# Optimization experiments

Hardware: AMD Instinct MI355X
Metric: run time of the kernel (lower is better)

## Reference

```python
import jax, jax.numpy as jnp
import numpy as np

KSIZE = 3
KN = (KSIZE - 1) // 2  # 1
TEMP = 50.0


def _extract_patches(x, same_pad):
    """TF tf.image.extract_patches ordering: per location, (dy, dx, channel).
    x: [b,H,W,d] -> [b,h,w,9*d] (h=H,w=W if same_pad else H-2,W-2)."""
    if same_pad:
        x = jnp.pad(x, ((0, 0), (KN, KN), (KN, KN), (0, 0)))
    b, Hp, Wp, d = x.shape
    h, w = Hp - 2 * KN, Wp - 2 * KN
    slices = [x[:, dy:dy + h, dx:dx + w, :]
              for dy in range(KSIZE) for dx in range(KSIZE)]
    return jnp.concatenate(slices, axis=-1)


def setup_inputs() -> dict:
    key = jax.random.key(0)
    k1, k2, k3 = jax.random.split(key, 3)
    b, h, w, dims = 4, 48, 48, 64
    g_in = jax.random.normal(k1, (b, h, w, dims), dtype=jnp.float32)
    # binary inpainting mask (1 = known background, 0 = hole)
    mask = (jax.random.uniform(k2, (b, h, w, 1)) > 0.5).astype(jnp.float32)
    W2 = jax.random.normal(k3, (2 * dims, dims), dtype=jnp.float32) / np.sqrt(2.0 * dims)
    b2 = jnp.zeros((dims,), dtype=jnp.float32)
    return {"g_in": g_in, "mask": mask, "W2": W2, "b2": b2}


def reference(g_in, mask, W2, b2):
    b, h, w, dims = g_in.shape
    c = (h - 2 * KN) * (w - 2 * KN)

    mask_r = mask  # already (h,w,1); broadcasts over dims (== tile)
    bg = g_in * mask_r

    # p1: VALID 3x3 patches of bg -> dynamic kernels, [b, c, 9*dims]
    p1 = _extract_patches(bg, same_pad=False).reshape(b, c, KSIZE * KSIZE * dims)
    # p2: SAME 3x3 patches of g_in, [b, h, w, 9*dims]
    p2 = _extract_patches(g_in, same_pad=True)

    # cross-correlation: conv2d(ft, k1) == per-location dot with each bg patch
    CS = jnp.einsum('byxk,bjk->byxj', p2, p1)              # [b,h,w,c]
    k1d = jnp.sum(p1 * p1, axis=2)                          # [b,c]
    wwd = jnp.sum(p2 * p2, axis=3, keepdims=True)           # [b,h,w,1]
    DS1 = k1d[:, None, None, :] + wwd - 2.0 * CS            # squared distances
    mu = jnp.mean(DS1, axis=3, keepdims=True)
    sd = jnp.std(DS1, axis=3, keepdims=True)                # population std (tf.math.reduce_std)
    DS2 = -jnp.tanh((DS1 - mu) / sd)
    CA = jax.nn.softmax(TEMP * DS2, axis=-1)                # [b,h,w,c]

    # transposed conv aggregation with per-sample kernels k2[b,j,dy,dx,ch]
    k2 = p1.reshape(b, c, KSIZE, KSIZE, dims)
    CA_pad = jnp.pad(CA, ((0, 0), (KN, KN), (KN, KN), (0, 0)))
    acl = jnp.zeros((b, h, w, dims), dtype=g_in.dtype)
    for dy in range(KSIZE):
        for dx in range(KSIZE):
            win = CA_pad[:, 2 * KN - dy:2 * KN - dy + h, 2 * KN - dx:2 * KN - dx + w, :]
            acl = acl + jnp.einsum('byxj,bjd->byxd', win, k2[:, :, dy, dx, :])
    acl = acl / 9.0

    ACL = bg + acl * (1.0 - mask_r)
    con1 = jnp.concatenate([g_in, ACL], axis=3)             # [b,h,w,2*dims]
    return jax.nn.elu(jnp.einsum('byxk,kd->byxd', con1, W2) + b2)
```

## Files before the change

kernel.cpp:

```cpp
#include <hip/hip_runtime.h>
#include <hip/hip_fp16.h>
#include <math.h>

#define BB 4
#define HH 48
#define WW 48
#define DD 64
#define CH 46
#define CWp 46
#define CC (CH*CWp)
#define KK 576
#define HWp (HH*WW)
#define PW 50
#define PP (PW*PW)

#define SLOTW 48
#define NSLOT 2208
#define NGRP 276
#define KPAD NSLOT
#define KSPLIT0 1120
#define QW 2304
#define QROWS 2500

typedef __attribute__((ext_vector_type(8))) short short8;
typedef __attribute__((ext_vector_type(4))) float float4v;

#define OFFB_GPAD  ((size_t)0)
#define OFFB_BGPAD ((size_t)1280000)
#define OFFB_E     ((size_t)2560000)
#define OFFB_K1D   ((size_t)2596864)
#define OFFB_P1T   ((size_t)2632192)
#define OFFB_S     ((size_t)12806656)
#define OFFB_AGG0  ((size_t)53504512)
#define OFFB_AGG1  ((size_t)64121344)
#define OFFB_Q     ((size_t)74738176)

__device__ __forceinline__ ushort f2bf(float x) {
    unsigned u = __float_as_uint(x);
    return (ushort)((u + 0x7FFFu + ((u >> 16) & 1u)) >> 16);
}

__device__ __forceinline__ float waveReduceSum(float x) {
#pragma unroll
    for (int o = 32; o > 0; o >>= 1) x += __shfl_down(x, o, 64);
    return x;
}

__device__ __forceinline__ float blockReduce5(float x, float* sm) {
#pragma unroll
    for (int o = 32; o > 0; o >>= 1) x += __shfl_down(x, o, 64);
    int lane = threadIdx.x & 63, w = threadIdx.x >> 6;
    __syncthreads();
    if (lane == 0) sm[w] = x;
    __syncthreads();
    return sm[0] + sm[1] + sm[2] + sm[3] + sm[4];
}

__device__ __forceinline__ float fast_tanh(float z) {
    float e = __expf(2.f * z);
    return 1.f - 2.f / (e + 1.f);
}

typedef __attribute__((address_space(3))) void lds_void_t;
typedef __attribute__((address_space(1))) void gmem_void_t;
__device__ __forceinline__ void gld16(const ushort* g, ushort* lds) {
    __builtin_amdgcn_global_load_lds((gmem_void_t*)g, (lds_void_t*)lds, 16, 0, 0);
}

__global__ __launch_bounds__(256) void build_pads(const float* __restrict__ g,
                                                  const float* __restrict__ mask,
                                                  ushort* __restrict__ gpad,
                                                  ushort* __restrict__ bgpad,
                                                  float* __restrict__ e) {
    int w = threadIdx.x >> 6, c = threadIdx.x & 63;
    int q4 = blockIdx.x * 4 + w;
    int b = q4 / PP, q = q4 % PP;
    int yp = q / PW, xp = q % PW;
    size_t o = (size_t)q4 * DD + c;
    if (yp >= 1 && yp <= HH && xp >= 1 && xp <= WW) {
        int pix = (yp - 1) * WW + (xp - 1);
        float gv = g[((size_t)b * HWp + pix) * DD + c];
        float m  = mask[(size_t)b * HWp + pix];
        float bgv = gv * m;
        gpad[o]  = f2bf(gv);
        bgpad[o] = f2bf(bgv);
        float ss = waveReduceSum(bgv * bgv);
        if (c == 0) e[b * HWp + pix] = ss;
    } else {
        gpad[o] = 0;
        bgpad[o] = 0;
    }
}

__global__ __launch_bounds__(256) void build_p1t(const ushort* __restrict__ bgpad,
                                                 const float* __restrict__ e,
                                                 ushort* __restrict__ p1t,
                                                 float* __restrict__ k1d) {
    int d9 = blockIdx.y, b = blockIdx.z;
    int t = threadIdx.x;
    if (blockIdx.x == 35) {
        int jg = (b * 9 + d9) * 256 + t;
        if (jg < BB * NSLOT) {
            int bb = jg / NSLOT, st = jg - bb * NSLOT;
            int jy = st / SLOTW, jx = st - jy * SLOTW;
            float s = 0.f;
            if (jx < CWp) {
                const float* eb = e + bb * HWp + jy * WW + jx;
#pragma unroll
                for (int ddy = 0; ddy < 3; ddy++)
#pragma unroll
                    for (int ddx = 0; ddx < 3; ddx++) s += eb[ddy * WW + ddx];
            }
            k1d[jg] = s;
        }
        return;
    }
    __shared__ ushort T[64 * 65];
    int jt = blockIdx.x;
    int dy = d9 / 3, dx = d9 - dy * 3;
    const ushort* src = bgpad + (size_t)b * PP * DD;
    int lr = t >> 3, c8 = (t & 7) * 8;
#pragma unroll
    for (int pass = 0; pass < 2; pass++) {
        int r = lr + pass * 32;
        int st = jt * 64 + r;
        int jy = st / SLOTW, jx = st - jy * SLOTW;
        uint4 d = make_uint4(0, 0, 0, 0);
        if (jx < CWp && jy < CWp)
            d = *(const uint4*)(src + (size_t)((jy + dy + 1) * PW + (jx + dx + 1)) * DD + c8);
        ushort tmp[8];
        *(uint4*)tmp = d;
#pragma unroll
        for (int u = 0; u < 8; u++) T[r * 65 + c8 + u] = tmp[u];
    }
    __syncthreads();
#pragma unroll
    for (int pass = 0; pass < 2; pass++) {
        int c = lr + pass * 32;
        int j8 = (t & 7) * 8;
        int col0 = jt * 64 + j8;
        ushort tmp[8];
#pragma unroll
        for (int u = 0; u < 8; u++) tmp[u] = T[(j8 + u) * 65 + c];
        if (col0 < NSLOT)
            *(uint4*)(p1t + ((size_t)b * KK + d9 * 64 + c) * NSLOT + col0) = *(const uint4*)tmp;
    }
}

__global__ __launch_bounds__(256) void qgemm(const ushort* __restrict__ gpad,
                                             const ushort* __restrict__ bgpad,
                                             __half* __restrict__ Qout) {
    __shared__ ushort As[2 * 4096];
    __shared__ ushort Bs[2 * 4096];
    int i0 = blockIdx.x;
    int b = (i0 & 7) >> 1;
    int tile = ((i0 >> 3) << 1) | (i0 & 1);
    int ty = tile / 18, tx = tile - ty * 18;
    int m0 = ty * 128, n0 = tx * 128;
    const ushort* Ag = gpad + (size_t)b * PP * DD;
    const ushort* Bg = bgpad + (size_t)b * PP * DD;

    int tid = threadIdx.x;
    int l = tid & 63, w = tid >> 6;
    int quad = l >> 4, l15 = l & 15;
    int sw8 = (l15 >> 1) & 3;
    int wm = (w >> 1) * 64, wn = (w & 1) * 64;
    int rowInC = l >> 2;
    int cSw = (l & 3) ^ ((l >> 3) & 3);

#pragma unroll
    for (int i = 0; i < 2; i++) {
        int rg = w * 2 + i;
        int r = rg * 16 + rowInC;
        int u = m0 + r; if (u > QROWS - 1) u = QROWS - 1;
        int n = n0 + r;
        int vy = n / 48, vx = n - vy * 48;
        int baseA = u * DD + cSw * 8;
        int baseB = ((vy + 1) * PW + (vx + 1)) * DD + cSw * 8;
        gld16(Ag + baseA, As + rg * 512);
        gld16(Bg + baseB, Bs + rg * 512);
        gld16(Ag + baseA + 32, As + 4096 + rg * 512);
        gld16(Bg + baseB + 32, Bs + 4096 + rg * 512);
    }
    float4v acc[4][4];
#pragma unroll
    for (int i = 0; i < 4; i++)
#pragma unroll
        for (int j = 0; j < 4; j++) acc[i][j] = (float4v){0.f, 0.f, 0.f, 0.f};
    __syncthreads();
#pragma unroll
    for (int kb = 0; kb < 2; kb++) {
        const ushort* Ax = As + kb * 4096;
        const ushort* Bx = Bs + kb * 4096;
        short8 af[4], bf[4];
#pragma unroll
        for (int i = 0; i < 4; i++)
            af[i] = *(const short8*)&Ax[(wm + i * 16 + l15) * 32 + ((quad ^ sw8)) * 8];
#pragma unroll
        for (int j = 0; j < 4; j++)
            bf[j] = *(const short8*)&Bx[(wn + j * 16 + l15) * 32 + ((quad ^ sw8)) * 8];
#pragma unroll
        for (int i = 0; i < 4; i++)
#pragma unroll
            for (int j = 0; j < 4; j++)
                acc[i][j] = __builtin_amdgcn_mfma_f32_16x16x32_bf16(af[i], bf[j], acc[i][j], 0, 0, 0);
    }
    __half* C = Qout + (size_t)b * QROWS * QW;
#pragma unroll
    for (int i = 0; i < 4; i++) {
#pragma unroll
        for (int j = 0; j < 4; j++) {
            int n = n0 + wn + j * 16 + l15;
#pragma unroll
            for (int r = 0; r < 4; r++) {
                int m = m0 + wm + i * 16 + quad * 4 + r;
                if (m < QROWS) C[(size_t)m * QW + n] = __float2half(acc[i][j][r]);
            }
        }
    }
}

__device__ __forceinline__ void gather9(const __half* __restrict__ qb2,
                                        const float* __restrict__ k1,
                                        int g, float (&ds)[8], int& slot0, int& vc) {
    int jy = g / 6;
    int jxb = (g - jy * 6) * 8;
    slot0 = jy * SLOTW + jxb;
    vc = (jxb == 40) ? 6 : 8;
    float cs[8] = {0.f, 0.f, 0.f, 0.f, 0.f, 0.f, 0.f, 0.f};
    constexpr int UO[9] = {0, 1, 2, 50, 51, 52, 100, 101, 102};
    constexpr int VO[9] = {0, 1, 2, 48, 49, 50, 96, 97, 98};
#pragma unroll
    for (int s = 0; s < 9; s++) {
        const __half* p = qb2 + (size_t)UO[s] * QW + slot0;
        if ((VO[s] & 1) == 0) {
            uint4 d = *(const uint4*)(p + VO[s]);
            const __half2* h2 = (const __half2*)&d;
#pragma unroll
            for (int k = 0; k < 4; k++) {
                float2 f = __half22float2(h2[k]);
                cs[2 * k] += f.x; cs[2 * k + 1] += f.y;
            }
        } else {
            uint4 d = *(const uint4*)(p + VO[s] - 1);
            uint e2 = *(const uint*)(p + VO[s] + 7);
            uint wv[5] = {d.x, d.y, d.z, d.w, e2};
#pragma unroll
            for (int k = 0; k < 4; k++) {
                uint a = (wv[k] >> 16) | (wv[k + 1] << 16);
                __half2 h2 = *(__half2*)&a;
                float2 f = __half22float2(h2);
                cs[2 * k] += f.x; cs[2 * k + 1] += f.y;
            }
        }
    }
    float4 ka = *(const float4*)(k1 + slot0);
    float4 kb = *(const float4*)(k1 + slot0 + 4);
    float kk[8] = {ka.x, ka.y, ka.z, ka.w, kb.x, kb.y, kb.z, kb.w};
#pragma unroll
    for (int u = 0; u < 8; u++) ds[u] = kk[u] - 2.f * cs[u];
}

__global__ __launch_bounds__(320) void qrowsoft(const __half* __restrict__ Q,
                                                const float* __restrict__ k1d,
                                                ushort* __restrict__ CA) {
    __shared__ float sm[5];
    int i0 = blockIdx.x;
    int b = (i0 & 7) >> 1;
    int yx = ((i0 >> 3) << 1) | (i0 & 1);
    int y = yx / WW, x = yx - y * WW;
    size_t row = (size_t)b * HWp + yx;
    const __half* qb2 = Q + ((size_t)b * QROWS + y * PW + x) * QW;
    const float* k1 = k1d + (size_t)b * NSLOT;
    ushort* wout = CA + row * (size_t)NSLOT;

    int t = threadIdx.x;
    bool act = (t < NGRP);
    int slot0 = 0, vc = 0;
    float ds[8] = {0.f, 0.f, 0.f, 0.f, 0.f, 0.f, 0.f, 0.f};
    if (act) gather9(qb2, k1, t, ds, slot0, vc);

    float sum = 0.f;
#pragma unroll
    for (int u = 0; u < 8; u++) if (u < vc) sum += ds[u];
    sum = blockReduce5(sum, sm);
    float mu = sum / (float)CC;

    float vs = 0.f;
#pragma unroll
    for (int u = 0; u < 8; u++) if (u < vc) { float d = ds[u] - mu; vs += d * d; }
    vs = blockReduce5(vs, sm);
    float inv_sd = 1.f / sqrtf(vs / (float)CC);

    float es = 0.f;
#pragma unroll
    for (int u = 0; u < 8; u++) {
        ds[u] = (u < vc) ? __expf(-50.f * fast_tanh((ds[u] - mu) * inv_sd)) : 0.f;
        es += ds[u];
    }
    es = blockReduce5(es, sm);
    float invz = 1.f / es;

    if (act) {
        ushort o[8];
#pragma unroll
        for (int u = 0; u < 8; u++) o[u] = f2bf(ds[u] * invz);
        *(uint4*)(wout + slot0) = *(const uint4*)o;
    }
}

template <int NF, bool NMASK>
__device__ __forceinline__ void gemm_tile_db(const ushort* __restrict__ Ab,
                                             const ushort* __restrict__ Bb,
                                             int lda, int ldb, int kb, int ke,
                                             int Nrem,
                                             ushort* As, ushort* Bs,
                                             float4v (&acc)[4][NF]) {
    constexpr int NBI = NF / 2;
    constexpr int BBUF = 2048 * NBI;
    int tid = threadIdx.x;
    int l = tid & 63, w = tid >> 6;
    int quad = l >> 4, l15 = l & 15;
    int sw8 = (l15 >> 1) & 3;
    int wm = (w >> 1) * 64, wn = (w & 1) * (NF * 16);
    int rowInC = l >> 2;
    int cSw = (l & 3) ^ ((l >> 3) & 3);

#pragma unroll
    for (int i = 0; i < 2; i++) {
        int rg = w * 2 + i;
        gld16(Ab + (size_t)(rg * 16 + rowInC) * lda + kb + cSw * 8, As + rg * 512);
    }
#pragma unroll
    for (int i = 0; i < NBI; i++) {
        int rg = w * NBI + i;
        int r = rg * 16 + rowInC;
        if (!NMASK || r < Nrem)
            gld16(Bb + (size_t)r * ldb + kb + cSw * 8, Bs + rg * 512);
    }

    int buf = 0;
    for (int k0 = kb; k0 < ke; k0 += 32) {
        __syncthreads();
        int nb = buf ^ 1;
        if (k0 + 32 < ke) {
#pragma unroll
            for (int i = 0; i < 2; i++) {
                int rg = w * 2 + i;
                gld16(Ab + (size_t)(rg * 16 + rowInC) * lda + (k0 + 32) + cSw * 8,
                      As + nb * 4096 + rg * 512);
            }
#pragma unroll
            for (int i = 0; i < NBI; i++) {
                int rg = w * NBI + i;
                int r = rg * 16 + rowInC;
                if (!NMASK || r < Nrem)
                    gld16(Bb + (size_t)r * ldb + (k0 + 32) + cSw * 8,
                          Bs + nb * BBUF + rg * 512);
            }
        }
        const ushort* Ax = As + buf * 4096;
        const ushort* Bx = Bs + buf * BBUF;
        short8 af[4], bf[NF];
#pragma unroll
        for (int i = 0; i < 4; i++)
            af[i] = *(const short8*)&Ax[(wm + i * 16 + l15) * 32 + ((quad ^ sw8)) * 8];
#pragma unroll
        for (int j = 0; j < NF; j++)
            bf[j] = *(const short8*)&Bx[(wn + j * 16 + l15) * 32 + ((quad ^ sw8)) * 8];
#pragma unroll
        for (int i = 0; i < 4; i++)
#pragma unroll
            for (int j = 0; j < NF; j++)
                acc[i][j] = __builtin_amdgcn_mfma_f32_16x16x32_bf16(af[i], bf[j], acc[i][j], 0, 0, 0);
        buf = nb;
    }
}

__global__ __launch_bounds__(256) void gemm2_split(const ushort* __restrict__ A,
                                                   const ushort* __restrict__ Bt,
                                                   __half* __restrict__ agg0,
                                                   __half* __restrict__ agg1) {
    __shared__ ushort As[2 * 4096];
    __shared__ ushort Bs[2 * 6144];
    int i0 = blockIdx.x;
    int z = i0 & 7;
    int b = z >> 1, split = z & 1;
    int tile = i0 >> 3;
    int ty = tile / 3, tx = tile - ty * 3;
    int m0 = ty * 128, n0 = tx * 192;
    const ushort* Ab = A + (size_t)b * HWp * KPAD + (size_t)m0 * KPAD;
    const ushort* Bb = Bt + (size_t)b * KK * KPAD + (size_t)n0 * KPAD;
    float4v acc[4][6];
#pragma unroll
    for (int i = 0; i < 4; i++)
#pragma unroll
        for (int j = 0; j < 6; j++) acc[i][j] = (float4v){0.f, 0.f, 0.f, 0.f};

    gemm_tile_db<6, false>(Ab, Bb, KPAD, KPAD, split ? KSPLIT0 : 0,
                           split ? KPAD : KSPLIT0, 192, As, Bs, acc);

    int tid = threadIdx.x;
    int lane = tid & 63, wid = tid >> 6;
    int quad = lane >> 4, l15 = lane & 15;
    int wm = (wid >> 1) * 64, wn = (wid & 1) * 96;
    __half* C = (split ? agg1 : agg0) + (size_t)b * HWp * KK;
#pragma unroll
    for (int i = 0; i < 4; i++) {
#pragma unroll
        for (int j = 0; j < 6; j++) {
            int n = n0 + wn + j * 16 + l15;
#pragma unroll
            for (int r = 0; r < 4; r++) {
                int m = m0 + wm + i * 16 + quad * 4 + r;
                C[(size_t)m * KK + n] = __float2half(acc[i][j][r]);
            }
        }
    }
}

__global__ __launch_bounds__(256) void final_k(const float* __restrict__ g,
                                               const float* __restrict__ mask,
                                               const __half* __restrict__ agg0,
                                               const __half* __restrict__ agg1,
                                               const float* __restrict__ W2,
                                               const float* __restrict__ b2,
                                               float* __restrict__ out) {
    int w = threadIdx.x >> 6, d = threadIdx.x & 63;
    int pix = blockIdx.x * 4 + w;
    int b = pix / HWp, yx = pix % HWp;
    int y = yx / WW, x = yx % WW;

    __shared__ float con1[4][128];
    float acl = 0.f;
#pragma unroll
    for (int dy = 0; dy < 3; dy++) {
#pragma unroll
        for (int dx = 0; dx < 3; dx++) {
            int yy = y + 1 - dy, xx = x + 1 - dx;
            if (yy >= 0 && yy < HH && xx >= 0 && xx < WW) {
                size_t off = ((size_t)(b * HWp + yy * WW + xx)) * KK + (dy * 3 + dx) * DD + d;
                acl += __half2float(agg0[off]) + __half2float(agg1[off]);
            }
        }
    }
    float m = mask[pix];
    float gv = g[(size_t)pix * DD + d];
    float bgv = gv * m;
    float ACL = bgv + (acl / 9.f) * (1.f - m);
    con1[w][d] = gv;
    con1[w][64 + d] = ACL;
    __syncthreads();
    float accv = b2[d];
#pragma unroll 8
    for (int k = 0; k < 128; k++) accv = fmaf(con1[w][k], W2[k * 64 + d], accv);
    out[(size_t)pix * DD + d] = accv > 0.f ? accv : expm1f(accv);
}

extern "C" void kernel_launch(void* const* d_in, const int* in_sizes, int n_in,
                              void* d_out, int out_size, void* d_ws, size_t ws_size,
                              hipStream_t stream) {
    const float* g    = (const float*)d_in[0];
    const float* mask = (const float*)d_in[1];
    const float* W2   = (const float*)d_in[2];
    const float* b2   = (const float*)d_in[3];
    float* out = (float*)d_out;
    char* ws = (char*)d_ws;

    ushort* gpad  = (ushort*)(ws + OFFB_GPAD);
    ushort* bgpad = (ushort*)(ws + OFFB_BGPAD);
    float*  e     = (float*) (ws + OFFB_E);
    float*  k1d   = (float*) (ws + OFFB_K1D);
    ushort* p1t   = (ushort*)(ws + OFFB_P1T);
    ushort* CA    = (ushort*)(ws + OFFB_S);
    __half* agg0  = (__half*)(ws + OFFB_AGG0);
    __half* agg1  = (__half*)(ws + OFFB_AGG1);
    __half* Qbuf  = (__half*)(ws + OFFB_Q);

    build_pads<<<BB * PP / 4, 256, 0, stream>>>(g, mask, gpad, bgpad, e);
    build_p1t<<<dim3(36, 9, BB), 256, 0, stream>>>(bgpad, e, p1t, k1d);

    qgemm<<<1440, 256, 0, stream>>>(gpad, bgpad, Qbuf);
    qrowsoft<<<BB * HWp, 320, 0, stream>>>(Qbuf, k1d, CA);

    gemm2_split<<<432, 256, 0, stream>>>(CA, p1t, agg0, agg1);

    final_k<<<BB * HWp / 4, 256, 0, stream>>>(g, mask, agg0, agg1, W2, b2, out);
}
```

Before: 192.5 us.

## Process eight pixels per block in softmax kernel with shared Q row reuse

Replaces the per-pixel qrowsoft kernel with qrowsoft2, which handles eight horizontally adjacent output pixels per block. Each loaded Q row now feeds several 3x3 window sums, cutting redundant global loads. The eight reductions are batched into one shared-memory pass, the variance comes from a single-pass E[x^2]-mu^2 form, and the 9-tap sums are accumulated in half2. It also uses packed bf16 conversion and a cheaper softmax exp form. In exchange it uses more registers and shared memory, and fp16 accumulation plus single-pass variance could lose precision.

```diff
diff --git a/kernel.cpp b/kernel.cpp
--- a/kernel.cpp
+++ b/kernel.cpp
@@ -46,19 +46,21 @@
     return x;
 }
 
-__device__ __forceinline__ float blockReduce5(float x, float* sm) {
-#pragma unroll
-    for (int o = 32; o > 0; o >>= 1) x += __shfl_down(x, o, 64);
-    int lane = threadIdx.x & 63, w = threadIdx.x >> 6;
-    __syncthreads();
-    if (lane == 0) sm[w] = x;
-    __syncthreads();
-    return sm[0] + sm[1] + sm[2] + sm[3] + sm[4];
-}
-
-__device__ __forceinline__ float fast_tanh(float z) {
-    float e = __expf(2.f * z);
-    return 1.f - 2.f / (e + 1.f);
+__device__ __forceinline__ __half2 u2h2(uint u) {
+    union { uint u; __half2 h; } c; c.u = u; return c.h;
+}
+
+__device__ __forceinline__ uint cvtpk_bf16(float lo, float hi) {
+    uint r;
+    asm("v_cvt_pk_bf16_f32 %0, %1, %2" : "=v"(r) : "v"(lo), "v"(hi));
+    return r;
+}
+
+__device__ __forceinline__ float softexp(float d, float mu, float isd) {
+    float z = (d - mu) * isd;
+    float E2 = __expf(z + z);
+    float r = __builtin_amdgcn_rcpf(E2 + 1.f);
+    return __expf(fmaf(100.f, r, -50.f));
 }
 
 typedef __attribute__((address_space(3))) void lds_void_t;
@@ -220,92 +222,162 @@
     }
 }
 
-__device__ __forceinline__ void gather9(const __half* __restrict__ qb2,
-                                        const float* __restrict__ k1,
-                                        int g, float (&ds)[8], int& slot0, int& vc) {
-    int jy = g / 6;
-    int jxb = (g - jy * 6) * 8;
-    slot0 = jy * SLOTW + jxb;
-    vc = (jxb == 40) ? 6 : 8;
-    float cs[8] = {0.f, 0.f, 0.f, 0.f, 0.f, 0.f, 0.f, 0.f};
-    constexpr int UO[9] = {0, 1, 2, 50, 51, 52, 100, 101, 102};
-    constexpr int VO[9] = {0, 1, 2, 48, 49, 50, 96, 97, 98};
-#pragma unroll
-    for (int s = 0; s < 9; s++) {
-        const __half* p = qb2 + (size_t)UO[s] * QW + slot0;
-        if ((VO[s] & 1) == 0) {
-            uint4 d = *(const uint4*)(p + VO[s]);
-            const __half2* h2 = (const __half2*)&d;
-#pragma unroll
-            for (int k = 0; k < 4; k++) {
-                float2 f = __half22float2(h2[k]);
-                cs[2 * k] += f.x; cs[2 * k + 1] += f.y;
-            }
-        } else {
-            uint4 d = *(const uint4*)(p + VO[s] - 1);
-            uint e2 = *(const uint*)(p + VO[s] + 7);
-            uint wv[5] = {d.x, d.y, d.z, d.w, e2};
-#pragma unroll
-            for (int k = 0; k < 4; k++) {
-                uint a = (wv[k] >> 16) | (wv[k + 1] << 16);
-                __half2 h2 = *(__half2*)&a;
-                float2 f = __half22float2(h2);
-                cs[2 * k] += f.x; cs[2 * k + 1] += f.y;
-            }
-        }
-    }
-    float4 ka = *(const float4*)(k1 + slot0);
-    float4 kb = *(const float4*)(k1 + slot0 + 4);
-    float kk[8] = {ka.x, ka.y, ka.z, ka.w, kb.x, kb.y, kb.z, kb.w};
-#pragma unroll
-    for (int u = 0; u < 8; u++) ds[u] = kk[u] - 2.f * cs[u];
-}
-
-__global__ __launch_bounds__(320) void qrowsoft(const __half* __restrict__ Q,
-                                                const float* __restrict__ k1d,
-                                                ushort* __restrict__ CA) {
-    __shared__ float sm[5];
+__global__ __launch_bounds__(320) void qrowsoft2(const __half* __restrict__ Q,
+                                                 const float* __restrict__ k1d,
+                                                 ushort* __restrict__ CA) {
+    __shared__ float red[16][321];
     int i0 = blockIdx.x;
-    int b = (i0 & 7) >> 1;
-    int yx = ((i0 >> 3) << 1) | (i0 & 1);
-    int y = yx / WW, x = yx - y * WW;
-    size_t row = (size_t)b * HWp + yx;
-    const __half* qb2 = Q + ((size_t)b * QROWS + y * PW + x) * QW;
-    const float* k1 = k1d + (size_t)b * NSLOT;
-    ushort* wout = CA + row * (size_t)NSLOT;
+    int z = i0 & 7;
+    int b = z >> 1;
+    int sub = ((i0 >> 3) << 1) | (i0 & 1);
+    int y = sub / 6, xt = sub - y * 6;
+    int x0 = xt * 8;
 
     int t = threadIdx.x;
     bool act = (t < NGRP);
-    int slot0 = 0, vc = 0;
-    float ds[8] = {0.f, 0.f, 0.f, 0.f, 0.f, 0.f, 0.f, 0.f};
-    if (act) gather9(qb2, k1, t, ds, slot0, vc);
-
-    float sum = 0.f;
-#pragma unroll
-    for (int u = 0; u < 8; u++) if (u < vc) sum += ds[u];
-    sum = blockReduce5(sum, sm);
-    float mu = sum / (float)CC;
-
-    float vs = 0.f;
-#pragma unroll
-    for (int u = 0; u < 8; u++) if (u < vc) { float d = ds[u] - mu; vs += d * d; }
-    vs = blockReduce5(vs, sm);
-    float inv_sd = 1.f / sqrtf(vs / (float)CC);
-
-    float es = 0.f;
-#pragma unroll
-    for (int u = 0; u < 8; u++) {
-        ds[u] = (u < vc) ? __expf(-50.f * fast_tanh((ds[u] - mu) * inv_sd)) : 0.f;
-        es += ds[u];
-    }
-    es = blockReduce5(es, sm);
-    float invz = 1.f / es;
+    int jy = t / 6, jxb = (t - jy * 6) * 8;
+    int slot0 = jy * SLOTW + jxb;
+    bool vc6 = act && (jxb == 40);
+
+    __half2 acc[8][4];
+#pragma unroll
+    for (int p = 0; p < 8; p++)
+#pragma unroll
+        for (int k = 0; k < 4; k++) acc[p][k] = u2h2(0u);
+
+    float k1v[8] = {0.f, 0.f, 0.f, 0.f, 0.f, 0.f, 0.f, 0.f};
 
     if (act) {
-        ushort o[8];
-#pragma unroll
-        for (int u = 0; u < 8; u++) o[u] = f2bf(ds[u] * invz);
-        *(uint4*)(wout + slot0) = *(const uint4*)o;
+        const float* k1 = k1d + (size_t)b * NSLOT + slot0;
+        float4 ka = *(const float4*)k1;
+        float4 kb = *(const float4*)(k1 + 4);
+        k1v[0] = ka.x; k1v[1] = ka.y; k1v[2] = ka.z; k1v[3] = ka.w;
+        k1v[4] = kb.x; k1v[5] = kb.y; k1v[6] = kb.z; k1v[7] = kb.w;
+
+#pragma unroll 1
+        for (int dy = 0; dy < 3; dy++) {
+            const __half* rp = Q + ((size_t)b * QROWS + (size_t)(y + dy) * PW + x0) * QW
+                               + slot0 + dy * 48;
+            uint4 W4[10]; uint W1[10];
+#pragma unroll
+            for (int d = 0; d < 10; d++) {
+                const __half* pr = rp + (size_t)d * QW;
+                W4[d] = *(const uint4*)pr;
+                W1[d] = *(const uint*)(pr + 8);
+            }
+#pragma unroll
+            for (int d = 0; d < 10; d++) {
+                uint w0 = W4[d].x, w1 = W4[d].y, w2 = W4[d].z, w3 = W4[d].w, w4 = W1[d];
+                if (d < 8) {
+                    acc[d][0] = __hadd2(acc[d][0], u2h2(w0));
+                    acc[d][1] = __hadd2(acc[d][1], u2h2(w1));
+                    acc[d][2] = __hadd2(acc[d][2], u2h2(w2));
+                    acc[d][3] = __hadd2(acc[d][3], u2h2(w3));
+                }
+                if (d >= 1 && d <= 8) {
+                    uint s0 = (w0 >> 16) | (w1 << 16);
+                    uint s1 = (w1 >> 16) | (w2 << 16);
+                    uint s2 = (w2 >> 16) | (w3 << 16);
+                    uint s3 = (w3 >> 16) | (w4 << 16);
+                    acc[d-1][0] = __hadd2(acc[d-1][0], u2h2(s0));
+                    acc[d-1][1] = __hadd2(acc[d-1][1], u2h2(s1));
+                    acc[d-1][2] = __hadd2(acc[d-1][2], u2h2(s2));
+                    acc[d-1][3] = __hadd2(acc[d-1][3], u2h2(s3));
+                }
+                if (d >= 2) {
+                    acc[d-2][0] = __hadd2(acc[d-2][0], u2h2(w1));
+                    acc[d-2][1] = __hadd2(acc[d-2][1], u2h2(w2));
+                    acc[d-2][2] = __hadd2(acc[d-2][2], u2h2(w3));
+                    acc[d-2][3] = __hadd2(acc[d-2][3], u2h2(w4));
+                }
+            }
+        }
+    }
+
+    if (vc6) {
+#pragma unroll
+        for (int p = 0; p < 8; p++) acc[p][3] = u2h2(0u);
+    }
+
+#pragma unroll
+    for (int p = 0; p < 8; p++) {
+        float s1p = 0.f, s2p = 0.f;
+#pragma unroll
+        for (int k = 0; k < 4; k++) {
+            float2 f = __half22float2(acc[p][k]);
+            float d0 = k1v[2*k]   - 2.f * f.x;
+            float d1 = k1v[2*k+1] - 2.f * f.y;
+            s1p += d0 + d1;
+            s2p = fmaf(d0, d0, fmaf(d1, d1, s2p));
+        }
+        red[p][t] = s1p;
+        red[8 + p][t] = s2p;
+    }
+    __syncthreads();
+    if (t < 256) {
+        int v = t >> 4, sb = t & 15;
+        float s = 0.f;
+#pragma unroll
+        for (int k = 0; k < 20; k++) s += red[v][sb + 16 * k];
+#pragma unroll
+        for (int o = 8; o > 0; o >>= 1) s += __shfl_down(s, o, 16);
+        if (sb == 0) red[v][320] = s;
+    }
+    __syncthreads();
+    float mu[8], isd[8];
+#pragma unroll
+    for (int p = 0; p < 8; p++) {
+        float m = red[p][320] * (1.f / (float)CC);
+        float ex2 = red[8 + p][320] * (1.f / (float)CC);
+        mu[p] = m;
+        isd[p] = rsqrtf(ex2 - m * m);
+    }
+
+    uint eb[8][4];
+#pragma unroll
+    for (int p = 0; p < 8; p++) {
+        float es = 0.f;
+#pragma unroll
+        for (int k = 0; k < 4; k++) {
+            float2 f = __half22float2(acc[p][k]);
+            float d0 = k1v[2*k]   - 2.f * f.x;
+            float d1 = k1v[2*k+1] - 2.f * f.y;
+            if (k == 3 && vc6) { d0 = 1e9f; d1 = 1e9f; }
+            float e0 = softexp(d0, mu[p], isd[p]);
+            float e1 = softexp(d1, mu[p], isd[p]);
+            es += e0 + e1;
+            eb[p][k] = cvtpk_bf16(e0, e1);
+        }
+        red[p][t] = act ? es : 0.f;
+    }
+    __syncthreads();
+    if (t < 128) {
+        int v = t >> 4, sb = t & 15;
+        float s = 0.f;
+#pragma unroll
+        for (int k = 0; k < 20; k++) s += red[v][sb + 16 * k];
+#pragma unroll
+        for (int o = 8; o > 0; o >>= 1) s += __shfl_down(s, o, 16);
+        if (sb == 0) red[v][320] = s;
+    }
+    __syncthreads();
+
+    if (act) {
+#pragma unroll
+        for (int p = 0; p < 8; p++) {
+            float iz = __builtin_amdgcn_rcpf(red[p][320]);
+            uint o[4];
+#pragma unroll
+            for (int k = 0; k < 4; k++) {
+                uint w = eb[p][k];
+                float lo = __uint_as_float(w << 16) * iz;
+                float hi = __uint_as_float(w & 0xffff0000u) * iz;
+                o[k] = cvtpk_bf16(lo, hi);
+            }
+            int pix = y * WW + x0 + p;
+            ushort* wp = CA + ((size_t)b * HWp + pix) * (size_t)NSLOT + slot0;
+            *(uint4*)wp = *(const uint4*)o;
+        }
     }
 }
 
@@ -481,7 +553,7 @@
     build_p1t<<<dim3(36, 9, BB), 256, 0, stream>>>(bgpad, e, p1t, k1d);
 
     qgemm<<<1440, 256, 0, stream>>>(gpad, bgpad, Qbuf);
-    qrowsoft<<<BB * HWp, 320, 0, stream>>>(Qbuf, k1d, CA);
+    qrowsoft2<<<BB * HWp / 8, 320, 0, stream>>>(Qbuf, k1d, CA);
 
     gemm2_split<<<432, 256, 0, stream>>>(CA, p1t, agg0, agg1);
 
```

Measured after the change: 182.2 us. -5.3%, faster.
